# Optimization experiments

Hardware: AMD Instinct MI355X
Metric: run time of the kernel (lower is better)

## Reference

```python
import jax, jax.numpy as jnp
import numpy as np

B, S, D, H = 4, 4096, 1024, 64


def setup_inputs() -> dict:
    key = jax.random.key(0)
    k1, k2, k3, k4 = jax.random.split(key, 4)
    x = jax.random.normal(k1, (B, S, D), dtype=jnp.float32)
    # nn.Linear(D, H, bias=False) weights, stored as [D, H] for x @ W
    scale = 1.0 / np.sqrt(D)
    Wk = jax.random.uniform(k2, (D, H), dtype=jnp.float32, minval=-scale, maxval=scale)
    Wq = jax.random.uniform(k3, (D, H), dtype=jnp.float32, minval=-scale, maxval=scale)
    Wv = jax.random.uniform(k4, (D, H), dtype=jnp.float32, minval=-scale, maxval=scale)
    return {"x": x, "Wq": Wq, "Wk": Wk, "Wv": Wv}


def reference(x, Wq, Wk, Wv):
    # x: [B, S, D]
    head_size = Wq.shape[-1]
    q = jnp.einsum('bsd,dh->bsh', x, Wq)
    k = jnp.einsum('bsd,dh->bsh', x, Wk)
    v = jnp.einsum('bsd,dh->bsh', x, Wv)
    scores = jnp.einsum('bqh,bkh->bqk', q, k) * (head_size ** -0.5)  # [B,S,S]
    S_ = x.shape[1]
    causal = jnp.tril(jnp.ones((S_, S_), dtype=bool))
    scores = jnp.where(causal[None, :, :], scores, -jnp.inf)
    attn = jax.nn.softmax(scores, axis=-1)
    return jnp.einsum('bqk,bkh->bqh', attn, v)  # [B,S,H]
```

## Files before the change

kernel.cpp:

```cpp
#include <hip/hip_runtime.h>

typedef __attribute__((ext_vector_type(8))) short bf16x8;
typedef __attribute__((ext_vector_type(4))) float f32x4;

#define MFMA16(A, Bv, C) __builtin_amdgcn_mfma_f32_16x16x32_bf16((A), (Bv), (C), 0, 0, 0)
#define WAITVM(N) asm volatile("s_waitcnt vmcnt(" #N ")" ::: "memory")

static constexpr int NB = 4, NS = 4096, ND = 1024, NH = 64;

__device__ __forceinline__ unsigned short f2bf(float f) {
    union { float f; unsigned int u; } x; x.f = f;
    unsigned int r = x.u + 0x7fffu + ((x.u >> 16) & 1u);
    return (unsigned short)(r >> 16);
}

__device__ __forceinline__ void gload_lds16(const void* g, void* l) {
    __builtin_amdgcn_global_load_lds((const __attribute__((address_space(1))) void*)g,
                                     (__attribute__((address_space(3))) void*)l, 16, 0, 0);
}

__global__ __launch_bounds__(256) void wconv(
    const float* __restrict__ Wq, const float* __restrict__ Wk,
    const float* __restrict__ Wv, unsigned short* __restrict__ wT)
{
    int mn = blockIdx.x;
    int m = mn >> 6, n = mn & 63;
    const float* W = (m == 0) ? Wq : (m == 1) ? Wk : Wv;
    unsigned short* dst = wT + (size_t)mn * ND;
    for (int k = threadIdx.x; k < ND; k += 256)
        dst[k] = f2bf(W[(size_t)k * NH + n]);
}

__global__ __launch_bounds__(512) void qkv_proj(
    const float* __restrict__ x, const unsigned short* __restrict__ wT,
    unsigned short* __restrict__ qo, unsigned short* __restrict__ ko,
    unsigned short* __restrict__ vt)
{
    __shared__ unsigned short Ws[3][192][64];
    __shared__ float Xs[3][64][64];
    __shared__ unsigned short Ls[64][72];

    const int tid  = threadIdx.x;
    const int lane = tid & 63;
    const int w    = tid >> 6;
    const int lr   = lane & 15;
    const int lg   = lane >> 4;
    const int mg   = w >> 2;
    const int cg   = w & 3;
    const int mbase = blockIdx.x * 64;

    const int wr8 = lane >> 3;
    const int wck = (lane & 7) ^ wr8;
    const int xr4 = lane >> 4;
    const int xck = lane & 15;

    f32x4 acc[6];
    #pragma unroll
    for (int i = 0; i < 6; ++i) acc[i] = (f32x4){0.f, 0.f, 0.f, 0.f};

    #define STAGE(slot, kb)                                                           \
        do {                                                                          \
            _Pragma("unroll")                                                         \
            for (int i_ = 0; i_ < 3; ++i_) {                                          \
                int rb_ = w * 24 + i_ * 8;                                            \
                gload_lds16(wT + (size_t)(rb_ + wr8) * ND + (kb) + wck * 8,           \
                            &Ws[slot][rb_][0]);                                       \
            }                                                                         \
            _Pragma("unroll")                                                         \
            for (int j_ = 0; j_ < 2; ++j_) {                                          \
                int rb_ = w * 8 + j_ * 4;                                             \
                int r7_ = (rb_ + xr4) & 7;                                            \
                gload_lds16(x + (size_t)(mbase + rb_ + xr4) * ND + (kb)               \
                                + (xck ^ (r7_ << 1)) * 4,                             \
                            &Xs[slot][rb_][0]);                                       \
            }                                                                         \
        } while (0)

    STAGE(0, 0);
    STAGE(1, 64);

    for (int kt = 0; kt < 16; ++kt) {
        __builtin_amdgcn_sched_barrier(0);
        if (kt < 15) WAITVM(5);
        else         WAITVM(0);
        __builtin_amdgcn_s_barrier();
        __builtin_amdgcn_sched_barrier(0);
        if (kt + 2 < 16) STAGE((kt + 2) % 3, (kt + 2) * 64);
        __builtin_amdgcn_sched_barrier(0);

        const int slot = kt % 3;
        #pragma unroll
        for (int sub = 0; sub < 2; ++sub) {
            bf16x8 bfr[3];
            #pragma unroll
            for (int f = 0; f < 3; ++f) {
                int row = cg * 48 + f * 16 + lr;
                bfr[f] = *(const bf16x8*)&Ws[slot][row][(((sub << 2) | lg) ^ (lr & 7)) * 8];
            }
            #pragma unroll
            for (int a = 0; a < 2; ++a) {
                int row = mg * 32 + a * 16 + lr;
                const float* xp =
                    &Xs[slot][row][((((sub << 3) | (lg << 1)) ^ ((lr & 7) << 1))) * 4];
                float4 u0 = *(const float4*)xp;
                float4 u1 = *(const float4*)(xp + 4);
                bf16x8 af;
                af[0] = (short)f2bf(u0.x); af[1] = (short)f2bf(u0.y);
                af[2] = (short)f2bf(u0.z); af[3] = (short)f2bf(u0.w);
                af[4] = (short)f2bf(u1.x); af[5] = (short)f2bf(u1.y);
                af[6] = (short)f2bf(u1.z); af[7] = (short)f2bf(u1.w);
                #pragma unroll
                for (int f = 0; f < 3; ++f)
                    acc[a * 3 + f] = MFMA16(af, bfr[f], acc[a * 3 + f]);
            }
        }
    }

    #pragma unroll
    for (int a = 0; a < 2; ++a)
        #pragma unroll
        for (int f = 0; f < 3; ++f) {
            int b16 = cg * 3 + f;
            int sel = b16 >> 2;
            int col = (b16 & 3) * 16 + lr;
            #pragma unroll
            for (int rr = 0; rr < 4; ++rr) {
                int mrow = mg * 32 + a * 16 + lg * 4 + rr;
                float v = acc[a * 3 + f][rr];
                if (sel == 0)
                    qo[(size_t)(mbase + mrow) * NH + col] = f2bf(v * 0.125f);
                else if (sel == 1)
                    ko[(size_t)(mbase + mrow) * NH + col] = f2bf(v);
                else
                    Ls[mrow][col] = f2bf(v);
            }
        }
    __syncthreads();
    {
        int h  = tid >> 3;
        int s8 = (tid & 7) * 8;
        unsigned short tmp[8];
        #pragma unroll
        for (int jj = 0; jj < 8; ++jj) tmp[jj] = Ls[s8 + jj][h];
        int b_ = mbase >> 12;
        int sb = (mbase & (NS - 1)) + s8;
        unsigned short* dst = vt + ((size_t)(b_ * NH + h)) * NS + sb;
        bf16x8 v0;
        #pragma unroll
        for (int jj = 0; jj < 8; ++jj) v0[jj] = (short)tmp[jj];
        *(bf16x8*)dst = v0;
    }
    #undef STAGE
}

__global__ __launch_bounds__(256) void attn_part(
    const unsigned short* __restrict__ q, const unsigned short* __restrict__ k,
    const unsigned short* __restrict__ vt, float* __restrict__ pO,
    float* __restrict__ pm, float* __restrict__ pl)
{
    __shared__ unsigned short Kt[2][64][64];
    __shared__ unsigned short Vt[2][64][64];
    __shared__ unsigned short Ps[4][16][72];

    const int bid = blockIdx.x;
    const int b = bid & 3;
    const int j = (bid >> 2) & 63;
    const int c = bid >> 8;
    if (c > (j >> 3)) return;
    const int ntile = (j + 1 - c * 8 < 8) ? (j + 1 - c * 8) : 8;
    const int tg0 = c * 8;

    const int tid  = threadIdx.x;
    const int lane = tid & 63;
    const int w    = tid >> 6;
    const int lr   = lane & 15;
    const int lg   = lane >> 4;
    const size_t bq = (size_t)b * NS;
    const int qb = j * 64;

    const int srow = lane >> 3;
    const int schk = (lane & 7) ^ srow;

    #define STAGEKV(buf, tg)                                                          \
        do {                                                                          \
            int kvb_ = (tg) * 64;                                                     \
            if (w < 2) {                                                              \
                _Pragma("unroll")                                                     \
                for (int i_ = 0; i_ < 4; ++i_) {                                      \
                    int rb_ = w * 32 + i_ * 8;                                        \
                    const unsigned short* src_ =                                      \
                        k + (bq + kvb_ + rb_ + srow) * NH + schk * 8;                 \
                    gload_lds16(src_, &Kt[buf][rb_][0]);                              \
                }                                                                     \
            } else {                                                                  \
                _Pragma("unroll")                                                     \
                for (int i_ = 0; i_ < 4; ++i_) {                                      \
                    int rb_ = (w - 2) * 32 + i_ * 8;                                  \
                    const unsigned short* src_ =                                      \
                        vt + ((size_t)(b * NH + rb_ + srow)) * NS + kvb_ + schk * 8;  \
                    gload_lds16(src_, &Vt[buf][rb_][0]);                              \
                }                                                                     \
            }                                                                         \
        } while (0)

    bf16x8 qf0, qf1;
    {
        const unsigned short* qp = q + (bq + qb + w * 16 + lr) * NH + lg * 8;
        qf0 = *(const bf16x8*)qp;
        qf1 = *(const bf16x8*)(qp + 32);
    }

    f32x4 O[4];
    #pragma unroll
    for (int i = 0; i < 4; ++i) O[i] = (f32x4){0.f, 0.f, 0.f, 0.f};
    float mrow = -3.0e38f, lsum = 0.f;

    STAGEKV(0, tg0);
    __syncthreads();

    int cur = 0;
    for (int t = 0; t < ntile; ++t) {
        const int tg = tg0 + t;
        STAGEKV(cur ^ 1, (t + 1 < ntile) ? tg + 1 : tg0);

        f32x4 sf[4];
        #pragma unroll
        for (int f = 0; f < 4; ++f) {
            f32x4 s = (f32x4){0.f, 0.f, 0.f, 0.f};
            int row = f * 16 + lr;
            bf16x8 kb0 = *(const bf16x8*)&Kt[cur][row][((lg    ) ^ (lr & 7)) * 8];
            bf16x8 kb1 = *(const bf16x8*)&Kt[cur][row][((lg + 4) ^ (lr & 7)) * 8];
            s = MFMA16(kb0, qf0, s);
            s = MFMA16(kb1, qf1, s);
            sf[f] = s;
        }

        if (tg == j) {
            #pragma unroll
            for (int f = 0; f < 4; ++f)
                #pragma unroll
                for (int r = 0; r < 4; ++r) {
                    int kvl = f * 16 + lg * 4 + r;
                    int ql  = w * 16 + lr;
                    if (kvl > ql) sf[f][r] = -3.0e38f;
                }
        }

        float pmx = fmaxf(fmaxf(fmaxf(sf[0][0], sf[0][1]), fmaxf(sf[0][2], sf[0][3])),
                          fmaxf(fmaxf(sf[1][0], sf[1][1]), fmaxf(sf[1][2], sf[1][3])));
        float pmx2 = fmaxf(fmaxf(fmaxf(sf[2][0], sf[2][1]), fmaxf(sf[2][2], sf[2][3])),
                           fmaxf(fmaxf(sf[3][0], sf[3][1]), fmaxf(sf[3][2], sf[3][3])));
        pmx = fmaxf(pmx, pmx2);
        pmx = fmaxf(pmx, __shfl_xor(pmx, 16));
        pmx = fmaxf(pmx, __shfl_xor(pmx, 32));
        float mnew = fmaxf(mrow, pmx);
        float corr = __expf(mrow - mnew);
        mrow = mnew;
        float rs = 0.f;
        #pragma unroll
        for (int f = 0; f < 4; ++f)
            #pragma unroll
            for (int r = 0; r < 4; ++r) {
                float p = __expf(sf[f][r] - mnew);
                sf[f][r] = p;
                rs += p;
            }
        rs += __shfl_xor(rs, 16);
        rs += __shfl_xor(rs, 32);
        lsum = lsum * corr + rs;
        #pragma unroll
        for (int hf = 0; hf < 4; ++hf) O[hf] *= corr;

        #pragma unroll
        for (int f = 0; f < 4; ++f)
            #pragma unroll
            for (int r = 0; r < 4; ++r)
                Ps[w][lr][f * 16 + lg * 4 + r] = f2bf(sf[f][r]);

        bf16x8 pb0 = *(const bf16x8*)&Ps[w][lr][lg * 8];
        bf16x8 pb1 = *(const bf16x8*)&Ps[w][lr][32 + lg * 8];

        #pragma unroll
        for (int hf = 0; hf < 4; ++hf) {
            int row = hf * 16 + lr;
            bf16x8 vb0 = *(const bf16x8*)&Vt[cur][row][((lg    ) ^ (lr & 7)) * 8];
            bf16x8 vb1 = *(const bf16x8*)&Vt[cur][row][((lg + 4) ^ (lr & 7)) * 8];
            O[hf] = MFMA16(vb0, pb0, O[hf]);
            O[hf] = MFMA16(vb1, pb1, O[hf]);
        }

        __syncthreads();
        cur ^= 1;
    }

    const int a8 = j >> 3, r8 = j & 7;
    const int pidx = b * 288 + (a8 + 1) * (4 * a8 + r8) + c;
    float* Po = pO + (size_t)pidx * 4096;
    #pragma unroll
    for (int hf = 0; hf < 4; ++hf)
        *(f32x4*)&Po[(w * 16 + lr) * 64 + hf * 16 + lg * 4] = O[hf];
    if (lane < 16) {
        pm[pidx * 64 + w * 16 + lane] = mrow;
        pl[pidx * 64 + w * 16 + lane] = lsum;
    }
    #undef STAGEKV
}

__global__ __launch_bounds__(256) void attn_merge(
    const float* __restrict__ pO, const float* __restrict__ pm,
    const float* __restrict__ pl, float* __restrict__ out)
{
    const int bid = blockIdx.x;
    const int b = bid & 3, j = bid >> 2;
    const int nch = (j >> 3) + 1;
    const int a8 = j >> 3, r8 = j & 7;
    const int pbase = b * 288 + (a8 + 1) * (4 * a8 + r8);
    const int tid = threadIdx.x;
    const int row = tid >> 2, hq = (tid & 3) * 16;

    float M = -3.0e38f, L = 0.f;
    f32x4 acc0 = {0,0,0,0}, acc1 = {0,0,0,0}, acc2 = {0,0,0,0}, acc3 = {0,0,0,0};
    for (int cc = 0; cc < nch; ++cc) {
        int pidx = pbase + cc;
        float mc = pm[pidx * 64 + row];
        float lc = pl[pidx * 64 + row];
        const f32x4* po = (const f32x4*)(pO + (size_t)pidx * 4096 + row * 64 + hq);
        float Mn = fmaxf(M, mc);
        float sO = __expf(M - Mn), sN = __expf(mc - Mn);
        L = L * sO + lc * sN;
        acc0 = acc0 * sO + po[0] * sN;
        acc1 = acc1 * sO + po[1] * sN;
        acc2 = acc2 * sO + po[2] * sN;
        acc3 = acc3 * sO + po[3] * sN;
        M = Mn;
    }
    float inv = 1.f / L;
    float* op = out + ((size_t)b * NS + (size_t)j * 64 + row) * NH + hq;
    *(f32x4*)(op + 0)  = acc0 * inv;
    *(f32x4*)(op + 4)  = acc1 * inv;
    *(f32x4*)(op + 8)  = acc2 * inv;
    *(f32x4*)(op + 12) = acc3 * inv;
}

extern "C" void kernel_launch(void* const* d_in, const int* in_sizes, int n_in,
                              void* d_out, int out_size, void* d_ws, size_t ws_size,
                              hipStream_t stream)
{
    const float* x  = (const float*)d_in[0];
    const float* Wq = (const float*)d_in[1];
    const float* Wk = (const float*)d_in[2];
    const float* Wv = (const float*)d_in[3];
    float* out = (float*)d_out;

    const size_t n = (size_t)NB * NS * NH;
    unsigned short* qb_ = (unsigned short*)d_ws;
    unsigned short* kb_ = qb_ + n;
    unsigned short* vT  = kb_ + n;
    unsigned short* wT  = vT + n;
    float* pO  = (float*)(wT + 192 * 1024);
    float* pm_ = pO + (size_t)1152 * 4096;
    float* pl_ = pm_ + 1152 * 64;

    wconv<<<dim3(192), dim3(256), 0, stream>>>(Wq, Wk, Wv, wT);
    qkv_proj<<<dim3(256), dim3(512), 0, stream>>>(x, wT, qb_, kb_, vT);
    attn_part<<<dim3(2048), dim3(256), 0, stream>>>(qb_, kb_, vT, pO, pm_, pl_);
    attn_merge<<<dim3(256), dim3(256), 0, stream>>>(pO, pm_, pl_, out);
}
```

Baseline: 68.91 us.

## Restructure QKV projection: register-staged bf16 X tile, 4 waves, double buffering

The QKV projection kernel drops from 512 to 256 threads, and each wave now computes all 64 rows against its 48 output columns. X is loaded into registers, converted to bf16 once, and stored to LDS in bf16. Previously each consuming wave redid the fp32-to-bf16 conversion on every LDS read. The three-stage async global_load_lds pipeline with manual vmcnt waits becomes a two-stage double buffer synchronised with __syncthreads. This cuts LDS footprint and repeated conversion work, at the cost of fewer waves to hide memory latency and a shallower prefetch.

```diff
diff --git a/kernel.cpp b/kernel.cpp
--- a/kernel.cpp
+++ b/kernel.cpp
@@ -4,7 +4,6 @@
 typedef __attribute__((ext_vector_type(4))) float f32x4;
 
 #define MFMA16(A, Bv, C) __builtin_amdgcn_mfma_f32_16x16x32_bf16((A), (Bv), (C), 0, 0, 0)
-#define WAITVM(N) asm volatile("s_waitcnt vmcnt(" #N ")" ::: "memory")
 
 static constexpr int NB = 4, NS = 4096, ND = 1024, NH = 64;
 
@@ -31,13 +30,13 @@
         dst[k] = f2bf(W[(size_t)k * NH + n]);
 }
 
-__global__ __launch_bounds__(512) void qkv_proj(
+__global__ __launch_bounds__(256) void qkv_proj(
     const float* __restrict__ x, const unsigned short* __restrict__ wT,
     unsigned short* __restrict__ qo, unsigned short* __restrict__ ko,
     unsigned short* __restrict__ vt)
 {
-    __shared__ unsigned short Ws[3][192][64];
-    __shared__ float Xs[3][64][64];
+    __shared__ unsigned short Ws[2][192][64];
+    __shared__ unsigned short Xs[2][64][64];
     __shared__ unsigned short Ls[64][72];
 
     const int tid  = threadIdx.x;
@@ -45,88 +44,102 @@
     const int w    = tid >> 6;
     const int lr   = lane & 15;
     const int lg   = lane >> 4;
-    const int mg   = w >> 2;
-    const int cg   = w & 3;
     const int mbase = blockIdx.x * 64;
 
     const int wr8 = lane >> 3;
     const int wck = (lane & 7) ^ wr8;
-    const int xr4 = lane >> 4;
-    const int xck = lane & 15;
-
-    f32x4 acc[6];
+    const int xrow = tid & 63;
+    const int xch  = tid >> 6;
+    const int xc0  = ((xch * 2)     ^ (xrow & 7)) * 8;
+    const int xc1  = ((xch * 2 + 1) ^ (xrow & 7)) * 8;
+
+    f32x4 acc[4][3];
     #pragma unroll
-    for (int i = 0; i < 6; ++i) acc[i] = (f32x4){0.f, 0.f, 0.f, 0.f};
-
-    #define STAGE(slot, kb)                                                           \
-        do {                                                                          \
-            _Pragma("unroll")                                                         \
-            for (int i_ = 0; i_ < 3; ++i_) {                                          \
-                int rb_ = w * 24 + i_ * 8;                                            \
-                gload_lds16(wT + (size_t)(rb_ + wr8) * ND + (kb) + wck * 8,           \
-                            &Ws[slot][rb_][0]);                                       \
-            }                                                                         \
-            _Pragma("unroll")                                                         \
-            for (int j_ = 0; j_ < 2; ++j_) {                                          \
-                int rb_ = w * 8 + j_ * 4;                                             \
-                int r7_ = (rb_ + xr4) & 7;                                            \
-                gload_lds16(x + (size_t)(mbase + rb_ + xr4) * ND + (kb)               \
-                                + (xck ^ (r7_ << 1)) * 4,                             \
-                            &Xs[slot][rb_][0]);                                       \
-            }                                                                         \
+    for (int a = 0; a < 4; ++a)
+        #pragma unroll
+        for (int f = 0; f < 3; ++f) acc[a][f] = (f32x4){0.f, 0.f, 0.f, 0.f};
+
+    const float* xsrc = x + (size_t)(mbase + xrow) * ND + xch * 16;
+
+    #define STAGE_W(buf, kb)                                                         \
+        do {                                                                         \
+            _Pragma("unroll")                                                        \
+            for (int i_ = 0; i_ < 6; ++i_) {                                         \
+                int rb_ = w * 48 + i_ * 8;                                           \
+                gload_lds16(wT + (size_t)(rb_ + wr8) * ND + (kb) + wck * 8,          \
+                            &Ws[buf][rb_][0]);                                       \
+            }                                                                        \
         } while (0)
 
-    STAGE(0, 0);
-    STAGE(1, 64);
+    #define LOADX(kb)                                                                \
+        do {                                                                         \
+            xr0 = *(const float4*)(xsrc + (kb));                                     \
+            xr1 = *(const float4*)(xsrc + (kb) + 4);                                 \
+            xr2 = *(const float4*)(xsrc + (kb) + 8);                                 \
+            xr3 = *(const float4*)(xsrc + (kb) + 12);                                \
+        } while (0)
+
+    #define WRITEX(buf)                                                              \
+        do {                                                                         \
+            bf16x8 p0_, p1_;                                                         \
+            p0_[0] = (short)f2bf(xr0.x); p0_[1] = (short)f2bf(xr0.y);                \
+            p0_[2] = (short)f2bf(xr0.z); p0_[3] = (short)f2bf(xr0.w);                \
+            p0_[4] = (short)f2bf(xr1.x); p0_[5] = (short)f2bf(xr1.y);                \
+            p0_[6] = (short)f2bf(xr1.z); p0_[7] = (short)f2bf(xr1.w);                \
+            p1_[0] = (short)f2bf(xr2.x); p1_[1] = (short)f2bf(xr2.y);                \
+            p1_[2] = (short)f2bf(xr2.z); p1_[3] = (short)f2bf(xr2.w);                \
+            p1_[4] = (short)f2bf(xr3.x); p1_[5] = (short)f2bf(xr3.y);                \
+            p1_[6] = (short)f2bf(xr3.z); p1_[7] = (short)f2bf(xr3.w);                \
+            *(bf16x8*)&Xs[buf][xrow][xc0] = p0_;                                     \
+            *(bf16x8*)&Xs[buf][xrow][xc1] = p1_;                                     \
+        } while (0)
+
+    float4 xr0, xr1, xr2, xr3;
+    STAGE_W(0, 0);
+    LOADX(0);
+    WRITEX(0);
+    __syncthreads();
 
     for (int kt = 0; kt < 16; ++kt) {
-        __builtin_amdgcn_sched_barrier(0);
-        if (kt < 15) WAITVM(5);
-        else         WAITVM(0);
-        __builtin_amdgcn_s_barrier();
-        __builtin_amdgcn_sched_barrier(0);
-        if (kt + 2 < 16) STAGE((kt + 2) % 3, (kt + 2) * 64);
-        __builtin_amdgcn_sched_barrier(0);
-
-        const int slot = kt % 3;
-        #pragma unroll
-        for (int sub = 0; sub < 2; ++sub) {
+        const int cur = kt & 1;
+        if (kt + 1 < 16) {
+            STAGE_W(cur ^ 1, (kt + 1) * 64);
+            LOADX((kt + 1) * 64);
+        }
+
+        #pragma unroll
+        for (int kk = 0; kk < 2; ++kk) {
             bf16x8 bfr[3];
             #pragma unroll
             for (int f = 0; f < 3; ++f) {
-                int row = cg * 48 + f * 16 + lr;
-                bfr[f] = *(const bf16x8*)&Ws[slot][row][(((sub << 2) | lg) ^ (lr & 7)) * 8];
+                int row = w * 48 + f * 16 + lr;
+                bfr[f] = *(const bf16x8*)&Ws[cur][row][((kk * 4 + lg) ^ (lr & 7)) * 8];
             }
             #pragma unroll
-            for (int a = 0; a < 2; ++a) {
-                int row = mg * 32 + a * 16 + lr;
-                const float* xp =
-                    &Xs[slot][row][((((sub << 3) | (lg << 1)) ^ ((lr & 7) << 1))) * 4];
-                float4 u0 = *(const float4*)xp;
-                float4 u1 = *(const float4*)(xp + 4);
-                bf16x8 af;
-                af[0] = (short)f2bf(u0.x); af[1] = (short)f2bf(u0.y);
-                af[2] = (short)f2bf(u0.z); af[3] = (short)f2bf(u0.w);
-                af[4] = (short)f2bf(u1.x); af[5] = (short)f2bf(u1.y);
-                af[6] = (short)f2bf(u1.z); af[7] = (short)f2bf(u1.w);
+            for (int a = 0; a < 4; ++a) {
+                int row = a * 16 + lr;
+                bf16x8 af = *(const bf16x8*)&Xs[cur][row][((kk * 4 + lg) ^ (lr & 7)) * 8];
                 #pragma unroll
                 for (int f = 0; f < 3; ++f)
-                    acc[a * 3 + f] = MFMA16(af, bfr[f], acc[a * 3 + f]);
+                    acc[a][f] = MFMA16(af, bfr[f], acc[a][f]);
             }
         }
+
+        if (kt + 1 < 16) WRITEX(cur ^ 1);
+        __syncthreads();
     }
 
     #pragma unroll
-    for (int a = 0; a < 2; ++a)
+    for (int a = 0; a < 4; ++a)
         #pragma unroll
         for (int f = 0; f < 3; ++f) {
-            int b16 = cg * 3 + f;
+            int b16 = w * 3 + f;
             int sel = b16 >> 2;
             int col = (b16 & 3) * 16 + lr;
             #pragma unroll
             for (int rr = 0; rr < 4; ++rr) {
-                int mrow = mg * 32 + a * 16 + lg * 4 + rr;
-                float v = acc[a * 3 + f][rr];
+                int mrow = a * 16 + lg * 4 + rr;
+                float v = acc[a][f][rr];
                 if (sel == 0)
                     qo[(size_t)(mbase + mrow) * NH + col] = f2bf(v * 0.125f);
                 else if (sel == 1)
@@ -137,20 +150,23 @@
         }
     __syncthreads();
     {
-        int h  = tid >> 3;
-        int s8 = (tid & 7) * 8;
-        unsigned short tmp[8];
-        #pragma unroll
-        for (int jj = 0; jj < 8; ++jj) tmp[jj] = Ls[s8 + jj][h];
+        int h   = tid >> 2;
+        int s16 = (tid & 3) * 16;
+        unsigned short tmp[16];
+        #pragma unroll
+        for (int jj = 0; jj < 16; ++jj) tmp[jj] = Ls[s16 + jj][h];
         int b_ = mbase >> 12;
-        int sb = (mbase & (NS - 1)) + s8;
+        int sb = (mbase & (NS - 1)) + s16;
         unsigned short* dst = vt + ((size_t)(b_ * NH + h)) * NS + sb;
-        bf16x8 v0;
-        #pragma unroll
-        for (int jj = 0; jj < 8; ++jj) v0[jj] = (short)tmp[jj];
-        *(bf16x8*)dst = v0;
-    }
-    #undef STAGE
+        bf16x8 v0, v1;
+        #pragma unroll
+        for (int jj = 0; jj < 8; ++jj) { v0[jj] = (short)tmp[jj]; v1[jj] = (short)tmp[8 + jj]; }
+        *(bf16x8*)dst       = v0;
+        *(bf16x8*)(dst + 8) = v1;
+    }
+    #undef STAGE_W
+    #undef LOADX
+    #undef WRITEX
 }
 
 __global__ __launch_bounds__(256) void attn_part(
@@ -362,7 +378,7 @@
     float* pl_ = pm_ + 1152 * 64;
 
     wconv<<<dim3(192), dim3(256), 0, stream>>>(Wq, Wk, Wv, wT);
-    qkv_proj<<<dim3(256), dim3(512), 0, stream>>>(x, wT, qb_, kb_, vT);
+    qkv_proj<<<dim3(256), dim3(256), 0, stream>>>(x, wT, qb_, kb_, vT);
     attn_part<<<dim3(2048), dim3(256), 0, stream>>>(qb_, kb_, vT, pO, pm_, pl_);
     attn_merge<<<dim3(256), dim3(256), 0, stream>>>(pO, pm_, pl_, out);
 }
```

Measured after the change: 79.13 us. 1.15x slower.
